# Kernel optimization log

Hardware: AMD Instinct MI355X
Metric: run time of the kernel (lower is better)

## Reference

```python
import jax, jax.numpy as jnp
import numpy as np

B, C, H, W = 4, 256, 64, 64


def conv_bn_relu(x, w, b):
    # 3x3 conv, stride 1, pad 1 (SAME) + folded eval-mode BatchNorm (absorbed
    # into w, b as a per-channel affine) + ReLU.
    y = jax.lax.conv_general_dilated(
        x, w, window_strides=(1, 1), padding='SAME',
        dimension_numbers=('NCHW', 'OIHW', 'NCHW'))
    return jax.nn.relu(y + b[None, :, None, None])


def setup_inputs() -> dict:
    key = jax.random.key(0)
    ks = jax.random.split(key, 9)

    def wgt(k):
        return (jax.random.normal(k, (C, C, 3, 3), jnp.float32) * 0.02)

    def bias(k):
        return (jax.random.normal(jax.random.fold_in(k, 1), (C,), jnp.float32) * 0.02)

    return {
        'x': jax.random.normal(ks[0], (B, C, H, W), jnp.float32),
        'wq': wgt(ks[1]), 'bq': bias(ks[1]),
        'wk': wgt(ks[2]), 'bk': bias(ks[2]),
        'wv': wgt(ks[3]), 'bv': bias(ks[3]),
        'wo': wgt(ks[4]), 'bo': bias(ks[4]),
    }


def reference(x, wq, bq, wk, bk, wv, bv, wo, bo):
    b, c, h, w = x.shape
    n = h * w
    # gen_attmap: conv-BN-ReLU projections, flatten spatial dims
    q = conv_bn_relu(x, wq, bq).reshape(b, c, n)   # [B, C, N]
    k = conv_bn_relu(x, wk, bk).reshape(b, c, n)   # [B, C, N]
    v = conv_bn_relu(x, wv, bv).reshape(b, c, n)   # [B, C, N]
    # sim_map = softmax(Q^T K) over keys; context = sim_map @ V^T
    sim = jax.nn.softmax(jnp.einsum('bcn,bcm->bnm', q, k), axis=-1)  # [B, N, N]
    ctx = jnp.einsum('bnm,bcm->bcn', sim, v).reshape(b, c, h, w)
    # sub_factor == 1: the block-rearranged branch and the avg-pooled branch
    # are identical (rearrange, avgpool(1,1) and interpolate(scale=1) are all
    # identity), so x_div + x_avg == 2 * ctx.
    return conv_bn_relu(ctx + ctx, wo, bo)
```

## Files before the change

### kernel.cpp

```cpp
#include <hip/hip_runtime.h>
#include <hip/hip_fp16.h>
#include <math.h>

#define NN 4096
#define CC 256

typedef __attribute__((ext_vector_type(8))) short bf16x8;
typedef __attribute__((ext_vector_type(8))) _Float16 f16x8;
typedef __attribute__((ext_vector_type(4))) float f32x4;
typedef __attribute__((ext_vector_type(16))) float f32x16;
typedef __attribute__((ext_vector_type(8))) unsigned short u16x8;
typedef __attribute__((ext_vector_type(4))) unsigned short u16x4;
typedef __attribute__((ext_vector_type(4))) unsigned int u32x4;

__device__ inline unsigned short f2bf(float f) {
  unsigned u = __float_as_uint(f);
  return (unsigned short)((u + 0x7FFFu + ((u >> 16) & 1u)) >> 16);
}
__device__ inline float bf2f(unsigned short u) {
  return __uint_as_float(((unsigned)u) << 16);
}
__device__ inline unsigned short f2h(float f) {
  __half h = __float2half(f);
  return static_cast<__half_raw>(h).x;
}

__device__ inline void gload16(const void* g, void* l) {
  __builtin_amdgcn_global_load_lds(
      (const __attribute__((address_space(1))) void*)g,
      (__attribute__((address_space(3))) void*)l, 16, 0, 0);
}

__global__ __launch_bounds__(256) void prep_w(
    const float* __restrict__ w0, const float* __restrict__ w1,
    const float* __restrict__ w2, const float* __restrict__ w3,
    unsigned short* __restrict__ wT2, unsigned short* __restrict__ zp)
{
  int bx = blockIdx.x;
  int widx = bx >> 8;
  const float* src = (widx == 0) ? w0 : (widx == 1) ? w1 : (widx == 2) ? w2 : w3;
  int p = ((bx & 255) << 8) + threadIdx.x;
  unsigned short* dst = wT2 + (size_t)widx * 589824;
  const float* s9 = src + (size_t)p * 9;
#pragma unroll
  for (int s = 0; s < 9; ++s) dst[(size_t)s * 65536 + p] = f2bf(s9[s]);
  if (bx == 0 && threadIdx.x < 128) zp[threadIdx.x] = 0;
}

__global__ __launch_bounds__(256) void prep_x(
    const float* __restrict__ x, unsigned short* __restrict__ xT)
{
  __shared__ unsigned short T[64][72];
  int tid = threadIdx.x, bx = blockIdx.x;
  int b = bx >> 8, c0 = ((bx >> 6) & 3) * 64, n0 = (bx & 63) * 64;
#pragma unroll
  for (int it = 0; it < 16; ++it) {
    int c_l = (tid >> 6) + it * 4;
    int n_l = tid & 63;
    T[n_l][c_l] = f2bf(x[((size_t)(b * 256 + c0 + c_l)) * 4096 + n0 + n_l]);
  }
  __syncthreads();
#pragma unroll
  for (int it = 0; it < 8; ++it) {
    int n_l = (tid >> 5) + it * 8;
    int cp = (tid & 31) * 2;
    unsigned v = (unsigned)T[n_l][cp] | ((unsigned)T[n_l][cp + 1] << 16);
    *(unsigned*)&xT[((size_t)(b * 4096 + n0 + n_l)) * 256 + c0 + cp] = v;
  }
}

__global__ __launch_bounds__(256) void conv3x_k(
    const unsigned short* __restrict__ A,
    const unsigned short* __restrict__ wT2,
    const float* __restrict__ bq, const float* __restrict__ bk,
    const float* __restrict__ bvv,
    unsigned short* __restrict__ qT, unsigned short* __restrict__ kT,
    unsigned short* __restrict__ vTc,
    const unsigned short* __restrict__ zp)
{
  __shared__ unsigned short As[2][128 * 64];
  __shared__ unsigned short Bs[2][64 * 64];

  const int by = blockIdx.y;
  const unsigned short* W = wT2 + (size_t)by * 589824;
  const float* bias = (by == 0) ? bq : (by == 1) ? bk : bvv;
  unsigned short* outp = (by == 0) ? qT : (by == 1) ? kT : vTc;
  const int mode2 = (by == 2);

  const int bx = blockIdx.x;
  const int bxs = ((bx & 7) << 6) + (bx >> 3);
  const int tid = threadIdx.x;
  const int lane = tid & 63;
  const int w = tid >> 6;
  const int wr = w >> 1, wc = w & 1;
  const int nt = bxs & 3;
  const int mt = bxs >> 2;
  const int m0 = mt * 128;
  const int co0 = nt * 64;

  const int aslot = (lane & 7) ^ (lane >> 3);
  int gmj[4], yj[4], xj[4];
#pragma unroll
  for (int j = 0; j < 4; ++j) {
    int row = w * 32 + j * 8 + (lane >> 3);
    int gm = m0 + row;
    gmj[j] = gm;
    int n = gm & (NN - 1);
    yj[j] = n >> 6;
    xj[j] = n & 63;
  }
  int browj[2];
#pragma unroll
  for (int j = 0; j < 2; ++j)
    browj[j] = co0 + w * 16 + j * 8 + (lane >> 3);

  f32x4 acc[4][2];
#pragma unroll
  for (int mi = 0; mi < 4; ++mi)
#pragma unroll
    for (int ni = 0; ni < 2; ++ni) acc[mi][ni] = (f32x4){0.f, 0.f, 0.f, 0.f};

  auto stage = [&](int step, int sb) {
    int s = step >> 2, t = step & 3;
    int dy = s / 3 - 1, dx = s - (s / 3) * 3 - 1;
    const unsigned short* abase = A + t * 64 + aslot * 8;
    const unsigned short* wbase = W + ((size_t)s << 16) + t * 64 + aslot * 8;
#pragma unroll
    for (int j = 0; j < 4; ++j) {
      int yy = yj[j] + dy, xx = xj[j] + dx;
      bool valid = ((unsigned)yy < 64u) && ((unsigned)xx < 64u);
      const void* ga = valid
          ? (const void*)(abase + (size_t)(gmj[j] + dy * 64 + dx) * 256)
          : (const void*)zp;
      gload16(ga, (void*)&As[sb][(w * 4 + j) * 512]);
    }
#pragma unroll
    for (int j = 0; j < 2; ++j) {
      const void* gb = (const void*)(wbase + (size_t)browj[j] * 256);
      gload16(gb, (void*)&Bs[sb][(w * 2 + j) * 512]);
    }
  };

  const int r = lane & 15;
  const int klane = lane >> 4;
  const int rs = r & 7;

  int buf = 0;
  stage(0, 0);
  __syncthreads();
  for (int step = 0; step < 36; ++step) {
    if (step + 1 < 36) stage(step + 1, buf ^ 1);
    const unsigned short* as = As[buf];
    const unsigned short* bs = Bs[buf];
#pragma unroll
    for (int kk = 0; kk < 2; ++kk) {
      int slot = (kk * 4 + klane) ^ rs;
      bf16x8 a[4], bfr[2];
#pragma unroll
      for (int mi = 0; mi < 4; ++mi)
        a[mi] = *(const bf16x8*)&as[(wr * 64 + mi * 16 + r) * 64 + slot * 8];
#pragma unroll
      for (int ni = 0; ni < 2; ++ni)
        bfr[ni] = *(const bf16x8*)&bs[(wc * 32 + ni * 16 + r) * 64 + slot * 8];
#pragma unroll
      for (int mi = 0; mi < 4; ++mi)
#pragma unroll
        for (int ni = 0; ni < 2; ++ni)
          acc[mi][ni] = __builtin_amdgcn_mfma_f32_16x16x32_bf16(
              a[mi], bfr[ni], acc[mi][ni], 0, 0, 0);
    }
    __syncthreads();
    buf ^= 1;
  }

  const int r4 = lane >> 4;
  const int colb = lane & 15;
  if (!mode2) {
#pragma unroll
    for (int ni = 0; ni < 2; ++ni) {
      int co = co0 + wc * 32 + ni * 16 + colb;
      float bv = bias[co];
#pragma unroll
      for (int mi = 0; mi < 4; ++mi) {
        int gm0 = m0 + wr * 64 + mi * 16 + r4 * 4;
#pragma unroll
        for (int rr = 0; rr < 4; ++rr) {
          float v = fmaxf(acc[mi][ni][rr] + bv, 0.f);
          outp[(size_t)(gm0 + rr) * 256 + co] = f2h(v);
        }
      }
    }
  } else {
#pragma unroll
    for (int ni = 0; ni < 2; ++ni) {
      int co = co0 + wc * 32 + ni * 16 + colb;
      float bv = bias[co];
#pragma unroll
      for (int mi = 0; mi < 4; ++mi) {
        int gm0 = m0 + wr * 64 + mi * 16 + r4 * 4;
#pragma unroll
        for (int rr = 0; rr < 4; ++rr) {
          float v = fmaxf(acc[mi][ni][rr] + bv, 0.f);
          int gm = gm0 + rr;
          int b = gm >> 12, n = gm & (NN - 1);
          outp[((size_t)(b * 256 + co)) * 4096 + n] = f2h(v);
        }
      }
    }
  }
}

__global__ __launch_bounds__(256) void conv_mfma(
    const unsigned short* __restrict__ A,
    const unsigned short* __restrict__ W,
    const float* __restrict__ bias,
    float* __restrict__ out,
    const unsigned short* __restrict__ zp)
{
  __shared__ unsigned short As[2][128 * 64];
  __shared__ unsigned short Bs[2][64 * 64];

  const int bx = blockIdx.x;
  const int bxs = ((bx & 7) << 6) + (bx >> 3);
  const int tid = threadIdx.x;
  const int lane = tid & 63;
  const int w = tid >> 6;
  const int wr = w >> 1, wc = w & 1;
  const int nt = bxs & 3;
  const int mt = bxs >> 2;
  const int m0 = mt * 128;
  const int co0 = nt * 64;

  const int aslot = (lane & 7) ^ (lane >> 3);
  int gmj[4], yj[4], xj[4];
#pragma unroll
  for (int j = 0; j < 4; ++j) {
    int row = w * 32 + j * 8 + (lane >> 3);
    int gm = m0 + row;
    gmj[j] = gm;
    int n = gm & (NN - 1);
    yj[j] = n >> 6;
    xj[j] = n & 63;
  }
  int browj[2];
#pragma unroll
  for (int j = 0; j < 2; ++j)
    browj[j] = co0 + w * 16 + j * 8 + (lane >> 3);

  f32x4 acc[4][2];
#pragma unroll
  for (int mi = 0; mi < 4; ++mi)
#pragma unroll
    for (int ni = 0; ni < 2; ++ni) acc[mi][ni] = (f32x4){0.f, 0.f, 0.f, 0.f};

  auto stage = [&](int step, int sb) {
    int s = step >> 2, t = step & 3;
    int dy = s / 3 - 1, dx = s - (s / 3) * 3 - 1;
    const unsigned short* abase = A + t * 64 + aslot * 8;
    const unsigned short* wbase = W + ((size_t)s << 16) + t * 64 + aslot * 8;
#pragma unroll
    for (int j = 0; j < 4; ++j) {
      int yy = yj[j] + dy, xx = xj[j] + dx;
      bool valid = ((unsigned)yy < 64u) && ((unsigned)xx < 64u);
      const void* ga = valid
          ? (const void*)(abase + (size_t)(gmj[j] + dy * 64 + dx) * 256)
          : (const void*)zp;
      gload16(ga, (void*)&As[sb][(w * 4 + j) * 512]);
    }
#pragma unroll
    for (int j = 0; j < 2; ++j) {
      const void* gb = (const void*)(wbase + (size_t)browj[j] * 256);
      gload16(gb, (void*)&Bs[sb][(w * 2 + j) * 512]);
    }
  };

  const int r = lane & 15;
  const int klane = lane >> 4;
  const int rs = r & 7;

  int buf = 0;
  stage(0, 0);
  __syncthreads();
  for (int step = 0; step < 36; ++step) {
    if (step + 1 < 36) stage(step + 1, buf ^ 1);
    const unsigned short* as = As[buf];
    const unsigned short* bs = Bs[buf];
#pragma unroll
    for (int kk = 0; kk < 2; ++kk) {
      int slot = (kk * 4 + klane) ^ rs;
      bf16x8 a[4], bfr[2];
#pragma unroll
      for (int mi = 0; mi < 4; ++mi)
        a[mi] = *(const bf16x8*)&as[(wr * 64 + mi * 16 + r) * 64 + slot * 8];
#pragma unroll
      for (int ni = 0; ni < 2; ++ni)
        bfr[ni] = *(const bf16x8*)&bs[(wc * 32 + ni * 16 + r) * 64 + slot * 8];
#pragma unroll
      for (int mi = 0; mi < 4; ++mi)
#pragma unroll
        for (int ni = 0; ni < 2; ++ni)
          acc[mi][ni] = __builtin_amdgcn_mfma_f32_16x16x32_bf16(
              a[mi], bfr[ni], acc[mi][ni], 0, 0, 0);
    }
    __syncthreads();
    buf ^= 1;
  }

  const int r4 = lane >> 4;
  const int colb = lane & 15;
#pragma unroll
  for (int ni = 0; ni < 2; ++ni) {
    int co = co0 + wc * 32 + ni * 16 + colb;
    float bv = bias[co];
#pragma unroll
    for (int mi = 0; mi < 4; ++mi) {
      int gm0 = m0 + wr * 64 + mi * 16 + r4 * 4;
#pragma unroll
      for (int rr = 0; rr < 4; ++rr) {
        float v = fmaxf(acc[mi][ni][rr] + bv, 0.f);
        int gm = gm0 + rr;
        int b = gm >> 12, n = gm & (NN - 1);
        out[((size_t)(b * 256 + co)) * 4096 + n] = v;
      }
    }
  }
}

__global__ __launch_bounds__(256, 2) void attn_k(
    const unsigned short* __restrict__ qT, const unsigned short* __restrict__ kT,
    const unsigned short* __restrict__ vTc,
    unsigned short* __restrict__ pO, float2* __restrict__ pml)
{
  __shared__ unsigned short Ks[2][32 * 256];
  __shared__ unsigned short Vts[2][256 * 32];

  const int tid = threadIdx.x;
  const int lane = tid & 63;
  const int w = tid >> 6;
  const int wq = w >> 1, wc = w & 1;
  const int hi = lane >> 5;
  const int la = lane & 31;
  const int a7 = la & 7;
  const int bx = blockIdx.x;
  const int bxs = ((bx & 7) << 6) + (bx >> 3);
  const int half = bxs >> 8;
  const int b = (bxs >> 6) & 3;
  const int q0 = (bxs & 63) << 6;
  const int kbase = half << 11;

  f16x8 qf[16];
  {
    const unsigned short* qp =
        qT + ((size_t)(b * NN) + q0 + 32 * wq + la) * CC + 8 * hi;
#pragma unroll
    for (int ks = 0; ks < 16; ++ks)
      qf[ks] = *(const f16x8*)(qp + ks * 16);
  }

  const unsigned short* kTb = kT + (size_t)b * NN * CC;
  const unsigned short* vTb = vTc + (size_t)b * CC * NN;
  auto stageKV = [&](int t, int sb) {
    int k0 = kbase + (t << 5);
    {
      int row_l = lane >> 5;
      int slot = lane & 31;
#pragma unroll
      for (int i = 0; i < 4; ++i) {
        int row = 8 * w + i * 2 + row_l;
        const void* src = (const void*)(kTb + (size_t)(k0 + row) * CC +
                                        ((slot ^ (row & 7)) << 3));
        gload16(src, (void*)&Ks[sb][(8 * w + i * 2) * 256]);
      }
    }
    {
      int c_l = lane >> 2;
      int sp = lane & 3;
#pragma unroll
      for (int i = 0; i < 4; ++i) {
        int c = 64 * w + 16 * i + c_l;
        const void* src = (const void*)(vTb + (size_t)c * NN + k0 +
                                        ((sp ^ ((c >> 2) & 3)) << 3));
        gload16(src, (void*)&Vts[sb][(64 * w + 16 * i) * 32]);
      }
    }
  };

  float mprev = -INFINITY, lsum = 0.f;
  f32x16 O[4];
#pragma unroll
  for (int nc = 0; nc < 4; ++nc)
#pragma unroll
    for (int rr = 0; rr < 16; ++rr) O[nc][rr] = 0.f;

  stageKV(0, 0);
  __syncthreads();

  int buf = 0;
  for (int t = 0; t < 64; ++t) {
    if (t + 1 < 64) stageKV(t + 1, buf ^ 1);

    f32x16 S0;
#pragma unroll
    for (int rr = 0; rr < 16; ++rr) S0[rr] = 0.f;
    const unsigned short* ks_ = Ks[buf];
    __builtin_amdgcn_s_setprio(1);
#pragma unroll
    for (int ks = 0; ks < 16; ++ks) {
      f16x8 a0 = *(const f16x8*)&ks_[la * 256 + ((((ks << 1) + hi) ^ a7) << 3)];
      S0 = __builtin_amdgcn_mfma_f32_32x32x16_f16(a0, qf[ks], S0, 0, 0, 0);
    }
    __builtin_amdgcn_s_setprio(0);

    float mloc = S0[0];
#pragma unroll
    for (int rr = 1; rr < 16; ++rr) mloc = fmaxf(mloc, S0[rr]);
    {
      auto sw = __builtin_amdgcn_permlane32_swap(
          __float_as_uint(mloc), __float_as_uint(mloc), false, false);
      mloc = fmaxf(__uint_as_float(sw[0]), __uint_as_float(sw[1]));
    }
    if (!__all(mloc <= mprev + 8.f)) {
      float mnew = fmaxf(mprev, mloc);
      float sc = __expf(mprev - mnew);
      lsum *= sc;
#pragma unroll
      for (int nc = 0; nc < 4; ++nc)
#pragma unroll
        for (int rr = 0; rr < 16; ++rr) O[nc][rr] *= sc;
      mprev = mnew;
    }
    float rsm = 0.f;
#pragma unroll
    for (int rr = 0; rr < 16; ++rr) {
      S0[rr] = __expf(S0[rr] - mprev);
      rsm += S0[rr];
    }
    {
      auto sw = __builtin_amdgcn_permlane32_swap(
          __float_as_uint(rsm), __float_as_uint(rsm), false, false);
      rsm = __uint_as_float(sw[0]) + __uint_as_float(sw[1]);
    }
    lsum += rsm;

    f16x8 pf[2];
#pragma unroll
    for (int kk = 0; kk < 2; ++kk) {
      const int r0 = kk * 8;
      unsigned w0 = __builtin_bit_cast(unsigned,
          __builtin_amdgcn_cvt_pkrtz(S0[r0 + 0], S0[r0 + 1]));
      unsigned w1 = __builtin_bit_cast(unsigned,
          __builtin_amdgcn_cvt_pkrtz(S0[r0 + 2], S0[r0 + 3]));
      unsigned w2 = __builtin_bit_cast(unsigned,
          __builtin_amdgcn_cvt_pkrtz(S0[r0 + 4], S0[r0 + 5]));
      unsigned w3 = __builtin_bit_cast(unsigned,
          __builtin_amdgcn_cvt_pkrtz(S0[r0 + 6], S0[r0 + 7]));
      auto sA = __builtin_amdgcn_permlane32_swap(w0, w2, false, false);
      auto sB = __builtin_amdgcn_permlane32_swap(w1, w3, false, false);
      u32x4 fw;
      fw[0] = sA[0]; fw[1] = sB[0]; fw[2] = sA[1]; fw[3] = sB[1];
      pf[kk] = __builtin_bit_cast(f16x8, fw);
    }

    const unsigned short* vs_ = Vts[buf];
    __builtin_amdgcn_s_setprio(1);
#pragma unroll
    for (int kk = 0; kk < 2; ++kk) {
#pragma unroll
      for (int nc = 0; nc < 4; ++nc) {
        int c = 128 * wc + 32 * nc + la;
        f16x8 vf = *(const f16x8*)&vs_[c * 32 +
                                       ((((kk << 1) + hi) ^ ((c >> 2) & 3)) << 3)];
        O[nc] = __builtin_amdgcn_mfma_f32_32x32x16_f16(vf, pf[kk], O[nc], 0, 0, 0);
      }
    }
    __builtin_amdgcn_s_setprio(0);

    __syncthreads();
    buf ^= 1;
  }

  {
    int n = q0 + 32 * wq + la;
    unsigned short* dst = pO + (((size_t)(half * 4 + b)) * NN + n) * CC;
#pragma unroll
    for (int nc = 0; nc < 4; ++nc) {
#pragma unroll
      for (int tq = 0; tq < 4; ++tq) {
        int c0 = 128 * wc + 32 * nc + 8 * tq + 4 * hi;
        u16x4 pk;
        pk[0] = f2bf(O[nc][4 * tq + 0]);
        pk[1] = f2bf(O[nc][4 * tq + 1]);
        pk[2] = f2bf(O[nc][4 * tq + 2]);
        pk[3] = f2bf(O[nc][4 * tq + 3]);
        *(u16x4*)&dst[c0] = pk;
      }
    }
    if (wc == 0 && hi == 0)
      pml[(size_t)half * 4 * NN + (size_t)b * NN + n] =
          make_float2(mprev, lsum);
  }
}

__global__ __launch_bounds__(256) void combine_k(
    const unsigned short* __restrict__ pO, const float2* __restrict__ pml,
    unsigned short* __restrict__ ctx)
{
  int bx = blockIdx.x;
  int b = bx >> 6;
  int q = ((bx & 63) << 6) + (threadIdx.x >> 2);
  int c0 = (threadIdx.x & 3) << 6;
  size_t nidx = (size_t)b * NN + q;
  float2 ml0 = pml[nidx];
  float2 ml1 = pml[(size_t)4 * NN + nidx];
  float m = fmaxf(ml0.x, ml1.x);
  float w0 = __expf(ml0.x - m), w1 = __expf(ml1.x - m);
  float inv = 2.f / (ml0.y * w0 + ml1.y * w1);
  const unsigned short* p0 = pO + nidx * CC + c0;
  const unsigned short* p1 = pO + (size_t)4 * NN * CC + nidx * CC + c0;
  unsigned short* d = ctx + nidx * CC + c0;
#pragma unroll
  for (int j = 0; j < 8; ++j) {
    u16x8 a = *(const u16x8*)(p0 + j * 8);
    u16x8 bb = *(const u16x8*)(p1 + j * 8);
    u16x8 o;
#pragma unroll
    for (int e = 0; e < 8; ++e)
      o[e] = f2bf((bf2f(a[e]) * w0 + bf2f(bb[e]) * w1) * inv);
    *(u16x8*)(d + j * 8) = o;
  }
}

extern "C" void kernel_launch(void* const* d_in, const int* in_sizes, int n_in,
                              void* d_out, int out_size, void* d_ws, size_t ws_size,
                              hipStream_t stream) {
  const float* x  = (const float*)d_in[0];
  const float* wq = (const float*)d_in[1];
  const float* bq = (const float*)d_in[2];
  const float* wk = (const float*)d_in[3];
  const float* bk = (const float*)d_in[4];
  const float* wv = (const float*)d_in[5];
  const float* bv = (const float*)d_in[6];
  const float* wo = (const float*)d_in[7];
  const float* bo = (const float*)d_in[8];

  char* ws = (char*)d_ws;
  unsigned short* xT  = (unsigned short*)(ws);
  unsigned short* wT2 = (unsigned short*)(ws + 8388608);
  unsigned short* qT  = (unsigned short*)(ws + 13107200);
  unsigned short* kT  = (unsigned short*)(ws + 21495808);
  unsigned short* vTc = (unsigned short*)(ws + 29884416);
  unsigned short* ctx = (unsigned short*)(ws + 38273024);
  unsigned short* zp  = (unsigned short*)(ws + 46661632);
  unsigned short* pO  = (unsigned short*)(ws + 46662144);
  float2*         pml = (float2*)(ws + 63439360);

  prep_w<<<dim3(1024), 256, 0, stream>>>(wq, wk, wv, wo, wT2, zp);
  prep_x<<<dim3(1024), 256, 0, stream>>>(x, xT);
  conv3x_k<<<dim3(512, 3), 256, 0, stream>>>(xT, wT2, bq, bk, bv, qT, kT, vTc, zp);
  attn_k<<<dim3(512), 256, 0, stream>>>(qT, kT, vTc, pO, pml);
  combine_k<<<dim3(256), 256, 0, stream>>>(pO, pml, ctx);
  conv_mfma<<<dim3(512), 256, 0, stream>>>(ctx, wT2 + 3 * 589824, bo, (float*)d_out, zp);
}
```

Baseline: 254.6 us.

## Split attention keys into four partitions with 512-thread blocks

Each attention block now handles 128 queries with 8 waves over a quarter of the keys instead of 64 queries over half. This halves the K/V tile count per block and shares each staged tile across twice as many queries. The combine kernel merges four partial outputs using their max and sum values, and the now-dead xT and ctx buffers are reused for partial storage. The risks are extra partial-output traffic and a launch bound of (512, 4) that severely limits registers per thread, which could cause spilling of the Q fragments and accumulators.

New measurement: 445.1 us. 1.75x slower.

```diff
diff --git a/kernel.cpp b/kernel.cpp
--- a/kernel.cpp
+++ b/kernel.cpp
@@ -326,10 +326,12 @@
   }
 }
 
-__global__ __launch_bounds__(256, 2) void attn_k(
+__global__ __launch_bounds__(512, 4) void attn_k(
     const unsigned short* __restrict__ qT, const unsigned short* __restrict__ kT,
     const unsigned short* __restrict__ vTc,
-    unsigned short* __restrict__ pO, float2* __restrict__ pml)
+    unsigned short* __restrict__ pA, unsigned short* __restrict__ pB,
+    unsigned short* __restrict__ pC, unsigned short* __restrict__ pD,
+    float2* __restrict__ pml)
 {
   __shared__ unsigned short Ks[2][32 * 256];
   __shared__ unsigned short Vts[2][256 * 32];
@@ -343,10 +345,10 @@
   const int a7 = la & 7;
   const int bx = blockIdx.x;
   const int bxs = ((bx & 7) << 6) + (bx >> 3);
-  const int half = bxs >> 8;
-  const int b = (bxs >> 6) & 3;
-  const int q0 = (bxs & 63) << 6;
-  const int kbase = half << 11;
+  const int quarter = bxs >> 7;
+  const int b = (bxs >> 5) & 3;
+  const int q0 = (bxs & 31) << 7;
+  const int kbase = quarter << 10;
 
   f16x8 qf[16];
   {
@@ -365,22 +367,22 @@
       int row_l = lane >> 5;
       int slot = lane & 31;
 #pragma unroll
-      for (int i = 0; i < 4; ++i) {
-        int row = 8 * w + i * 2 + row_l;
+      for (int i = 0; i < 2; ++i) {
+        int row = 4 * w + i * 2 + row_l;
         const void* src = (const void*)(kTb + (size_t)(k0 + row) * CC +
                                         ((slot ^ (row & 7)) << 3));
-        gload16(src, (void*)&Ks[sb][(8 * w + i * 2) * 256]);
+        gload16(src, (void*)&Ks[sb][(4 * w + i * 2) * 256]);
       }
     }
     {
       int c_l = lane >> 2;
       int sp = lane & 3;
 #pragma unroll
-      for (int i = 0; i < 4; ++i) {
-        int c = 64 * w + 16 * i + c_l;
+      for (int i = 0; i < 2; ++i) {
+        int c = 32 * w + 16 * i + c_l;
         const void* src = (const void*)(vTb + (size_t)c * NN + k0 +
                                         ((sp ^ ((c >> 2) & 3)) << 3));
-        gload16(src, (void*)&Vts[sb][(64 * w + 16 * i) * 32]);
+        gload16(src, (void*)&Vts[sb][(32 * w + 16 * i) * 32]);
       }
     }
   };
@@ -396,8 +398,8 @@
   __syncthreads();
 
   int buf = 0;
-  for (int t = 0; t < 64; ++t) {
-    if (t + 1 < 64) stageKV(t + 1, buf ^ 1);
+  for (int t = 0; t < 32; ++t) {
+    if (t + 1 < 32) stageKV(t + 1, buf ^ 1);
 
     f32x16 S0;
 #pragma unroll
@@ -481,7 +483,9 @@
 
   {
     int n = q0 + 32 * wq + la;
-    unsigned short* dst = pO + (((size_t)(half * 4 + b)) * NN + n) * CC;
+    unsigned short* pOq = (quarter == 0) ? pA : (quarter == 1) ? pB
+                        : (quarter == 2) ? pC : pD;
+    unsigned short* dst = pOq + ((size_t)b * NN + n) * CC;
 #pragma unroll
     for (int nc = 0; nc < 4; ++nc) {
 #pragma unroll
@@ -496,37 +500,41 @@
       }
     }
     if (wc == 0 && hi == 0)
-      pml[(size_t)half * 4 * NN + (size_t)b * NN + n] =
-          make_float2(mprev, lsum);
+      pml[((size_t)quarter * 4 + b) * NN + n] = make_float2(mprev, lsum);
   }
 }
 
 __global__ __launch_bounds__(256) void combine_k(
-    const unsigned short* __restrict__ pO, const float2* __restrict__ pml,
-    unsigned short* __restrict__ ctx)
+    const unsigned short* __restrict__ p0, const unsigned short* __restrict__ p1,
+    const unsigned short* __restrict__ p2, const unsigned short* __restrict__ p3,
+    const float2* __restrict__ pml, unsigned short* __restrict__ ctx)
 {
   int bx = blockIdx.x;
-  int b = bx >> 6;
-  int q = ((bx & 63) << 6) + (threadIdx.x >> 2);
-  int c0 = (threadIdx.x & 3) << 6;
-  size_t nidx = (size_t)b * NN + q;
-  float2 ml0 = pml[nidx];
-  float2 ml1 = pml[(size_t)4 * NN + nidx];
-  float m = fmaxf(ml0.x, ml1.x);
+  int b = bx >> 7;
+  int q = ((bx & 127) << 5) + (threadIdx.x >> 3);
+  int c0 = (threadIdx.x & 7) << 5;
+  size_t nq = (size_t)b * NN + q;
+  float2 ml0 = pml[(size_t)(0 * 4 + b) * NN + q];
+  float2 ml1 = pml[(size_t)(1 * 4 + b) * NN + q];
+  float2 ml2 = pml[(size_t)(2 * 4 + b) * NN + q];
+  float2 ml3 = pml[(size_t)(3 * 4 + b) * NN + q];
+  float m = fmaxf(fmaxf(ml0.x, ml1.x), fmaxf(ml2.x, ml3.x));
   float w0 = __expf(ml0.x - m), w1 = __expf(ml1.x - m);
-  float inv = 2.f / (ml0.y * w0 + ml1.y * w1);
-  const unsigned short* p0 = pO + nidx * CC + c0;
-  const unsigned short* p1 = pO + (size_t)4 * NN * CC + nidx * CC + c0;
-  unsigned short* d = ctx + nidx * CC + c0;
-#pragma unroll
-  for (int j = 0; j < 8; ++j) {
-    u16x8 a = *(const u16x8*)(p0 + j * 8);
-    u16x8 bb = *(const u16x8*)(p1 + j * 8);
+  float w2 = __expf(ml2.x - m), w3 = __expf(ml3.x - m);
+  float inv = 2.f / (ml0.y * w0 + ml1.y * w1 + ml2.y * w2 + ml3.y * w3);
+  size_t base = nq * CC + c0;
+#pragma unroll
+  for (int j = 0; j < 4; ++j) {
+    u16x8 a0 = *(const u16x8*)(p0 + base + j * 8);
+    u16x8 a1 = *(const u16x8*)(p1 + base + j * 8);
+    u16x8 a2 = *(const u16x8*)(p2 + base + j * 8);
+    u16x8 a3 = *(const u16x8*)(p3 + base + j * 8);
     u16x8 o;
 #pragma unroll
     for (int e = 0; e < 8; ++e)
-      o[e] = f2bf((bf2f(a[e]) * w0 + bf2f(bb[e]) * w1) * inv);
-    *(u16x8*)(d + j * 8) = o;
+      o[e] = f2bf((bf2f(a0[e]) * w0 + bf2f(a1[e]) * w1 +
+                   bf2f(a2[e]) * w2 + bf2f(a3[e]) * w3) * inv);
+    *(u16x8*)(ctx + base + j * 8) = o;
   }
 }
 
@@ -551,13 +559,14 @@
   unsigned short* vTc = (unsigned short*)(ws + 29884416);
   unsigned short* ctx = (unsigned short*)(ws + 38273024);
   unsigned short* zp  = (unsigned short*)(ws + 46661632);
-  unsigned short* pO  = (unsigned short*)(ws + 46662144);
+  unsigned short* pO2 = (unsigned short*)(ws + 46662144);
+  unsigned short* pO3 = (unsigned short*)(ws + 55050752);
   float2*         pml = (float2*)(ws + 63439360);
 
   prep_w<<<dim3(1024), 256, 0, stream>>>(wq, wk, wv, wo, wT2, zp);
   prep_x<<<dim3(1024), 256, 0, stream>>>(x, xT);
   conv3x_k<<<dim3(512, 3), 256, 0, stream>>>(xT, wT2, bq, bk, bv, qT, kT, vTc, zp);
-  attn_k<<<dim3(512), 256, 0, stream>>>(qT, kT, vTc, pO, pml);
-  combine_k<<<dim3(256), 256, 0, stream>>>(pO, pml, ctx);
+  attn_k<<<dim3(512), 512, 0, stream>>>(qT, kT, vTc, xT, ctx, pO2, pO3, pml);
+  combine_k<<<dim3(512), 256, 0, stream>>>(xT, ctx, pO2, pO3, pml, ctx);
   conv_mfma<<<dim3(512), 256, 0, stream>>>(ctx, wT2 + 3 * 589824, bo, (float*)d_out, zp);
 }
```
